# Kernel optimization log

Hardware: AMD Instinct MI355X
Metric: run time of the kernel (lower is better)

## Reference

```python
import jax, jax.numpy as jnp
import numpy as np

CHANNELS = 64
WEIGHT_NUMS = [66 * 64, 64 * 64, 64]  # layer0 (C+2)->C, layer1 C->C, layer2 C->1
BIAS_NUMS = [64, 64, 1]
NUM_GEN_PARAMS = sum(WEIGHT_NUMS) + sum(BIAS_NUMS)  # 8513


def setup_inputs() -> dict:
    key = jax.random.key(0)
    k1, k2 = jax.random.split(key)
    N, C, H, W = 4, 64, 80, 200
    num_ins = 8  # instances per image -> M = 32 total
    M = N * num_ins
    x = jax.random.normal(k1, (N, C, H, W), dtype=jnp.float32)
    mask_head_params = jax.random.normal(k2, (M, NUM_GEN_PARAMS), dtype=jnp.float32) * 0.1
    return {"x": x, "mask_head_params": mask_head_params, "num_ins": num_ins}


def reference(x, mask_head_params, num_ins):
    N, C, H, W = x.shape
    ch = CHANNELS
    # compute_locations with stride=1 (stride//2 == 0); source bug divides the
    # whole tensor by W (locations[:1,:,:] /= W on a batch-1 tensor).
    xx, yy = jnp.meshgrid(jnp.arange(W, dtype=x.dtype), jnp.arange(H, dtype=x.dtype), indexing='xy')
    loc = jnp.stack([xx, yy], axis=0) / W  # [2, H, W]
    xa = jnp.concatenate([jnp.broadcast_to(loc[None], (N, 2, H, W)), x], axis=1)  # [N, C+2, H, W]
    feats = jnp.repeat(xa, num_ins, axis=0)  # [M, C+2, H, W] per-instance inputs
    M = feats.shape[0]
    # parse_dynamic_params: split generated params into per-layer weights/biases
    splits = np.cumsum(WEIGHT_NUMS + BIAS_NUMS)[:-1]
    w0, w1, w2, b0, b1, b2 = jnp.split(mask_head_params, splits, axis=1)
    w0 = w0.reshape(M, ch, ch + 2)
    w1 = w1.reshape(M, ch, ch)
    w2 = w2.reshape(M, 1, ch)
    b2 = b2 - 2.19  # mask bias shift (is_mask=True)
    # grouped 1x1 convs (groups=M) as per-instance GEMMs with ReLU between layers
    h = jax.nn.relu(jnp.einsum('mkc,mchw->mkhw', w0, feats) + b0[:, :, None, None])
    h = jax.nn.relu(jnp.einsum('mkc,mchw->mkhw', w1, h) + b1[:, :, None, None])
    out = jnp.einsum('mkc,mchw->mkhw', w2, h) + b2[:, :, None, None]
    return out.reshape(1, -1, H, W)  # [1, M*out_channels, H, W]
```

## Files before the change

### kernel.cpp

```cpp
#include <hip/hip_runtime.h>

typedef __attribute__((ext_vector_type(8)))  short    short8;
typedef __attribute__((ext_vector_type(4)))  short    s16x4;
typedef __attribute__((ext_vector_type(4)))  float    f32x4;
typedef __attribute__((ext_vector_type(4)))  unsigned uint4_;
typedef __attribute__((ext_vector_type(2)))  unsigned uint2_;

#define HW     16000
#define WWID   200
#define NPARAM 8513
#define PACK_STRIDE 6144

__device__ __forceinline__ unsigned pkbf2(float a, float b) {
    unsigned r;
    asm("v_cvt_pk_bf16_f32 %0, %1, %2" : "=v"(r) : "v"(a), "v"(b));
    return r;
}
__device__ __forceinline__ s16x4 mk4(unsigned a, unsigned b) {
    uint2_ u; u.x = a; u.y = b;
    return __builtin_bit_cast(s16x4, u);
}
__device__ __forceinline__ void mfma16(f32x4& acc, s16x4 a, s16x4 b) {
    asm("s_nop 2\n\tv_mfma_f32_16x16x16_bf16 %0, %1, %2, %0"
        : "+v"(acc) : "v"(a), "v"(b));
}

__device__ __forceinline__ float w0val(const float* pm, int k, int c) {
    if (c < 64)  return pm[k * 66 + c + 2];
    if (c == 64) return pm[k * 66 + 0];
    if (c == 65) return pm[k * 66 + 1];
    if (c == 66) return pm[8384 + k];
    return 0.0f;
}

__global__ __launch_bounds__(256) void pack_weights(
    const float* __restrict__ params, unsigned* __restrict__ wp)
{
    const int m   = blockIdx.x;
    const int tid = threadIdx.x;
    const float* pm = params + (size_t)m * NPARAM;
    unsigned* dst = wp + (size_t)m * PACK_STRIDE;

    if (blockIdx.y == 0) {
        const int l  = tid >> 2;
        const int i0 = (tid & 3) * 2;
        #pragma unroll
        for (int frag = 0; frag < 12; ++frag) {
            int ch = frag >> 2, kb = frag & 3;
            int k = kb * 16 + (l & 15);
            int c = ch * 32 + (l >> 4) * 8 + i0;
            dst[frag * 256 + tid] = pkbf2(w0val(pm, k, c), w0val(pm, k, c + 1));
        }
        float* fd = (float*)dst;
        if (tid < 64) {
            fd[5120 + tid] = pm[8448 + tid];
            fd[5184 + tid] = pm[8320 + tid];
        }
        if (tid == 0) fd[5248] = pm[8512];
    } else {
        #pragma unroll
        for (int i = tid; i < 2048; i += 256) {
            int f = i >> 7, r = i & 127;
            int l = r >> 1, d = i & 1;
            int kb = f >> 2, ks = f & 3;
            int row = kb * 16 + (l & 15);
            int col = ks * 16 + (l >> 4) * 4 + d * 2;
            const float* s = pm + 4224 + row * 64 + col;
            dst[3072 + i] = pkbf2(s[0], s[1]);
        }
    }
}

__global__ __launch_bounds__(512, 4) void condlane_reg(
    const float* __restrict__ x,
    const unsigned* __restrict__ wp,
    float* __restrict__ out,
    int num_ins)
{
    extern __shared__ char lds_[];
    char*  xt = lds_;
    float* sm = (float*)(lds_ + 32768);
    const int tid  = threadIdx.x;
    const int lane = tid & 63;
    const int wid  = tid >> 6;
    const int n    = blockIdx.y;
    const int pxg0 = blockIdx.x * 128;
    const int g    = (lane >> 4) & 3;
    const int px16 = lane & 15;

    {
        const int p   = tid & 127;
        const int sel = tid >> 7;
        const float* xp = x + (size_t)n * 64 * HW + (pxg0 + p);
        #pragma unroll
        for (int it = 0; it < 2; ++it) {
            int c0 = sel * 16 + it * 8;
            uint4_ d;
            d.x = pkbf2(xp[(size_t)(c0 + 0) * HW], xp[(size_t)(c0 + 1) * HW]);
            d.y = pkbf2(xp[(size_t)(c0 + 2) * HW], xp[(size_t)(c0 + 3) * HW]);
            d.z = pkbf2(xp[(size_t)(c0 + 4) * HW], xp[(size_t)(c0 + 5) * HW]);
            d.w = pkbf2(xp[(size_t)(c0 + 6) * HW], xp[(size_t)(c0 + 7) * HW]);
            *(uint4_*)(xt + ((p * 256 + c0 * 2) ^ ((p & 15) << 4))) = d;
        }
        const int pg = pxg0 + p;
        float lx = (float)(pg % WWID) * (1.0f / WWID);
        float ly = (float)(pg / WWID) * (1.0f / WWID);
        uint4_ cv;
        cv.x = (sel == 0) ? pkbf2(lx, ly)   : 0u;
        cv.y = (sel == 0) ? pkbf2(1.f, 0.f) : 0u;
        cv.z = 0u; cv.w = 0u;
        *(uint4_*)(xt + ((p * 256 + 128 + sel * 16) ^ ((p & 15) << 4))) = cv;
    }

    const int m = n * num_ins + wid;
    const unsigned* wm = wp + (size_t)m * PACK_STRIDE;
    const float*    fm = (const float*)wm;
    float* sw = sm + wid * 136;

    sw[lane]      = fm[5120 + lane];
    sw[64 + lane] = fm[5184 + lane];
    if (lane == 0) sw[128] = fm[5248];

    short8 w0f[3][4];
    s16x4  w1f4[4][4];
    #pragma unroll
    for (int ch = 0; ch < 3; ++ch)
        #pragma unroll
        for (int kb = 0; kb < 4; ++kb)
            w0f[ch][kb] = *(const short8*)(wm + (ch * 4 + kb) * 256 + lane * 4);
    #pragma unroll
    for (int kb = 0; kb < 4; ++kb)
        #pragma unroll
        for (int ks = 0; ks < 4; ++ks)
            w1f4[kb][ks] = *(const s16x4*)(wm + 3072 + (kb * 4 + ks) * 128 + lane * 2);

    __syncthreads();

    const int swz = px16 << 4;
    const float* swg = sw + g * 4;

    for (int s = 0; s < 8; ++s) {
        const int pxl = s * 16 + px16;
        short8 xf[3];
        #pragma unroll
        for (int ch = 0; ch < 3; ++ch)
            xf[ch] = *(const short8*)(xt + ((pxl * 256 + ch * 64 + g * 16) ^ swz));
        f32x4 zero4; zero4[0] = 0.f; zero4[1] = 0.f; zero4[2] = 0.f; zero4[3] = 0.f;
        f32x4 acc0[4];
        #pragma unroll
        for (int kb = 0; kb < 4; ++kb)
            acc0[kb] = __builtin_amdgcn_mfma_f32_16x16x32_bf16(w0f[0][kb], xf[0], zero4, 0, 0, 0);
        #pragma unroll
        for (int ch = 1; ch < 3; ++ch)
            #pragma unroll
            for (int kb = 0; kb < 4; ++kb)
                acc0[kb] = __builtin_amdgcn_mfma_f32_16x16x32_bf16(w0f[ch][kb], xf[ch], acc0[kb], 0, 0, 0);
        s16x4 hf[4];
        #pragma unroll
        for (int ks = 0; ks < 4; ++ks)
            hf[ks] = mk4(pkbf2(fmaxf(acc0[ks][0], 0.f), fmaxf(acc0[ks][1], 0.f)),
                         pkbf2(fmaxf(acc0[ks][2], 0.f), fmaxf(acc0[ks][3], 0.f)));
        f32x4 acc1[4];
        #pragma unroll
        for (int kb = 0; kb < 4; ++kb)
            acc1[kb] = *(const f32x4*)(swg + kb * 16);
        #pragma unroll
        for (int ks = 0; ks < 4; ++ks)
            #pragma unroll
            for (int kb = 0; kb < 4; ++kb)
                mfma16(acc1[kb], w1f4[kb][ks], hf[ks]);
        asm("s_nop 7\n\ts_nop 7"
            : "+v"(acc1[0]), "+v"(acc1[1]), "+v"(acc1[2]), "+v"(acc1[3]));
        float v = 0.f;
        #pragma unroll
        for (int kb = 0; kb < 4; ++kb) {
            f32x4 w2k = *(const f32x4*)(swg + 64 + kb * 16);
            #pragma unroll
            for (int r = 0; r < 4; ++r)
                v += w2k[r] * fmaxf(acc1[kb][r], 0.f);
        }
        v += __shfl_xor(v, 16);
        v += __shfl_xor(v, 32);
        if (lane < 16)
            out[(size_t)m * HW + pxg0 + s * 16 + lane] = v + (sw[128] - 2.19f);
    }
}

extern "C" void kernel_launch(void* const* d_in, const int* in_sizes, int n_in,
                              void* d_out, int out_size, void* d_ws, size_t ws_size,
                              hipStream_t stream) {
    const float* x      = (const float*)d_in[0];
    const float* params = (const float*)d_in[1];
    float* out          = (float*)d_out;

    const int N = in_sizes[0] / (64 * HW);
    const int M = in_sizes[1] / NPARAM;
    const int num_ins = M / N;

    pack_weights<<<dim3(M, 2), 256, 0, stream>>>(params, (unsigned*)d_ws);

    dim3 grid(HW / 128, N);
    condlane_reg<<<grid, 512, 37120, stream>>>(x, (const unsigned*)d_ws, out, num_ins);
}
```

Baseline: 28.78 us.

## Fold location/bias channels into small K=16 MFMA and shrink LDS tile

Drops the third 32-wide K chunk of layer 0, which held only the two coordinate channels and the bias. Those are now handled by four 16x16x16 MFMAs whose B operand (x/y location, 1.0) is built in registers each step. The x tile in LDS halves to 128 bytes per pixel with a narrower swizzle, and the packed weight layout shrinks to match. This cuts LDS footprint, LDS writes and layer-0 MFMA work, which may raise occupancy. The cost is extra nop padding and per-step coordinate arithmetic.

```diff
diff --git a/kernel.cpp b/kernel.cpp
--- a/kernel.cpp
+++ b/kernel.cpp
@@ -9,7 +9,7 @@
 #define HW     16000
 #define WWID   200
 #define NPARAM 8513
-#define PACK_STRIDE 6144
+#define PACK_STRIDE 4864
 
 __device__ __forceinline__ unsigned pkbf2(float a, float b) {
     unsigned r;
@@ -24,13 +24,9 @@
     asm("s_nop 2\n\tv_mfma_f32_16x16x16_bf16 %0, %1, %2, %0"
         : "+v"(acc) : "v"(a), "v"(b));
 }
-
-__device__ __forceinline__ float w0val(const float* pm, int k, int c) {
-    if (c < 64)  return pm[k * 66 + c + 2];
-    if (c == 64) return pm[k * 66 + 0];
-    if (c == 65) return pm[k * 66 + 1];
-    if (c == 66) return pm[8384 + k];
-    return 0.0f;
+__device__ __forceinline__ void mfma16c(f32x4& acc, s16x4 a, s16x4 b) {
+    asm("s_nop 7\n\tv_mfma_f32_16x16x16_bf16 %0, %1, %2, %0"
+        : "+v"(acc) : "v"(a), "v"(b));
 }
 
 __global__ __launch_bounds__(256) void pack_weights(
@@ -45,18 +41,32 @@
         const int l  = tid >> 2;
         const int i0 = (tid & 3) * 2;
         #pragma unroll
-        for (int frag = 0; frag < 12; ++frag) {
-            int ch = frag >> 2, kb = frag & 3;
+        for (int f = 0; f < 8; ++f) {
+            int ch = f >> 2, kb = f & 3;
             int k = kb * 16 + (l & 15);
             int c = ch * 32 + (l >> 4) * 8 + i0;
-            dst[frag * 256 + tid] = pkbf2(w0val(pm, k, c), w0val(pm, k, c + 1));
+            const float* s = pm + k * 66 + 2 + c;
+            dst[f * 256 + tid] = pkbf2(s[0], s[1]);
+        }
+        #pragma unroll
+        for (int it = 0; it < 2; ++it) {
+            int idx = it * 256 + tid;
+            int kb = idx >> 7, rem = idx & 127;
+            int ll = rem >> 1, d = rem & 1;
+            int gg = (ll >> 4) & 3;
+            int k = kb * 16 + (ll & 15);
+            unsigned v = 0u;
+            if (gg == 0)
+                v = d ? pkbf2(pm[8384 + k], 0.f)
+                      : pkbf2(pm[k * 66 + 0], pm[k * 66 + 1]);
+            dst[4096 + idx] = v;
         }
         float* fd = (float*)dst;
         if (tid < 64) {
-            fd[5120 + tid] = pm[8448 + tid];
-            fd[5184 + tid] = pm[8320 + tid];
-        }
-        if (tid == 0) fd[5248] = pm[8512];
+            fd[4608 + tid] = pm[8448 + tid];
+            fd[4672 + tid] = pm[8320 + tid];
+        }
+        if (tid == 0) fd[4736] = pm[8512];
     } else {
         #pragma unroll
         for (int i = tid; i < 2048; i += 256) {
@@ -66,7 +76,7 @@
             int row = kb * 16 + (l & 15);
             int col = ks * 16 + (l >> 4) * 4 + d * 2;
             const float* s = pm + 4224 + row * 64 + col;
-            dst[3072 + i] = pkbf2(s[0], s[1]);
+            dst[2048 + i] = pkbf2(s[0], s[1]);
         }
     }
 }
@@ -79,7 +89,7 @@
 {
     extern __shared__ char lds_[];
     char*  xt = lds_;
-    float* sm = (float*)(lds_ + 32768);
+    float* sm = (float*)(lds_ + 16384);
     const int tid  = threadIdx.x;
     const int lane = tid & 63;
     const int wid  = tid >> 6;
@@ -100,16 +110,8 @@
             d.y = pkbf2(xp[(size_t)(c0 + 2) * HW], xp[(size_t)(c0 + 3) * HW]);
             d.z = pkbf2(xp[(size_t)(c0 + 4) * HW], xp[(size_t)(c0 + 5) * HW]);
             d.w = pkbf2(xp[(size_t)(c0 + 6) * HW], xp[(size_t)(c0 + 7) * HW]);
-            *(uint4_*)(xt + ((p * 256 + c0 * 2) ^ ((p & 15) << 4))) = d;
-        }
-        const int pg = pxg0 + p;
-        float lx = (float)(pg % WWID) * (1.0f / WWID);
-        float ly = (float)(pg / WWID) * (1.0f / WWID);
-        uint4_ cv;
-        cv.x = (sel == 0) ? pkbf2(lx, ly)   : 0u;
-        cv.y = (sel == 0) ? pkbf2(1.f, 0.f) : 0u;
-        cv.z = 0u; cv.w = 0u;
-        *(uint4_*)(xt + ((p * 256 + 128 + sel * 16) ^ ((p & 15) << 4))) = cv;
+            *(uint4_*)(xt + ((p * 128 + c0 * 2) ^ ((p & 7) << 4))) = d;
+        }
     }
 
     const int m = n * num_ins + wid;
@@ -117,44 +119,65 @@
     const float*    fm = (const float*)wm;
     float* sw = sm + wid * 136;
 
-    sw[lane]      = fm[5120 + lane];
-    sw[64 + lane] = fm[5184 + lane];
-    if (lane == 0) sw[128] = fm[5248];
-
-    short8 w0f[3][4];
+    sw[lane]      = fm[4608 + lane];
+    sw[64 + lane] = fm[4672 + lane];
+    if (lane == 0) sw[128] = fm[4736];
+
+    short8 w0f[2][4];
     s16x4  w1f4[4][4];
+    s16x4  wloc[4];
     #pragma unroll
-    for (int ch = 0; ch < 3; ++ch)
+    for (int ch = 0; ch < 2; ++ch)
         #pragma unroll
         for (int kb = 0; kb < 4; ++kb)
             w0f[ch][kb] = *(const short8*)(wm + (ch * 4 + kb) * 256 + lane * 4);
     #pragma unroll
-    for (int kb = 0; kb < 4; ++kb)
+    for (int kb = 0; kb < 4; ++kb) {
         #pragma unroll
         for (int ks = 0; ks < 4; ++ks)
-            w1f4[kb][ks] = *(const s16x4*)(wm + 3072 + (kb * 4 + ks) * 128 + lane * 2);
+            w1f4[kb][ks] = *(const s16x4*)(wm + 2048 + (kb * 4 + ks) * 128 + lane * 2);
+        wloc[kb] = *(const s16x4*)(wm + 4096 + kb * 128 + lane * 2);
+    }
+
+    const int pxg00 = pxg0 + px16;
+    float colf = (float)(pxg00 % WWID);
+    float rowf = (float)(pxg00 / WWID);
+    const unsigned gmask = (g == 0) ? 0xFFFFFFFFu : 0u;
+    const unsigned lbv   = (g == 0) ? 0x00003f80u : 0u;
 
     __syncthreads();
 
-    const int swz = px16 << 4;
+    const int swz = (px16 & 7) << 4;
     const float* swg = sw + g * 4;
 
     for (int s = 0; s < 8; ++s) {
         const int pxl = s * 16 + px16;
-        short8 xf[3];
-        #pragma unroll
-        for (int ch = 0; ch < 3; ++ch)
-            xf[ch] = *(const short8*)(xt + ((pxl * 256 + ch * 64 + g * 16) ^ swz));
+        short8 xf[2];
+        #pragma unroll
+        for (int ch = 0; ch < 2; ++ch)
+            xf[ch] = *(const short8*)(xt + ((pxl * 128 + ch * 64 + g * 16) ^ swz));
         f32x4 zero4; zero4[0] = 0.f; zero4[1] = 0.f; zero4[2] = 0.f; zero4[3] = 0.f;
         f32x4 acc0[4];
         #pragma unroll
         for (int kb = 0; kb < 4; ++kb)
             acc0[kb] = __builtin_amdgcn_mfma_f32_16x16x32_bf16(w0f[0][kb], xf[0], zero4, 0, 0, 0);
         #pragma unroll
-        for (int ch = 1; ch < 3; ++ch)
+        for (int kb = 0; kb < 4; ++kb)
+            acc0[kb] = __builtin_amdgcn_mfma_f32_16x16x32_bf16(w0f[1][kb], xf[1], acc0[kb], 0, 0, 0);
+        {
+            float lx = colf * (1.0f / WWID);
+            float ly = rowf * (1.0f / WWID);
+            s16x4 locB = mk4(pkbf2(lx, ly) & gmask, lbv);
             #pragma unroll
             for (int kb = 0; kb < 4; ++kb)
-                acc0[kb] = __builtin_amdgcn_mfma_f32_16x16x32_bf16(w0f[ch][kb], xf[ch], acc0[kb], 0, 0, 0);
+                mfma16c(acc0[kb], wloc[kb], locB);
+            colf += 16.f;
+            bool wrap = colf >= (float)WWID;
+            colf = wrap ? colf - (float)WWID : colf;
+            rowf = wrap ? rowf + 1.f : rowf;
+        }
+        asm("s_nop 7\n\ts_nop 7"
+            : "+v"(acc0[0]), "+v"(acc0[1]), "+v"(acc0[2]), "+v"(acc0[3]));
         s16x4 hf[4];
         #pragma unroll
         for (int ks = 0; ks < 4; ++ks)
@@ -200,5 +223,5 @@
     pack_weights<<<dim3(M, 2), 256, 0, stream>>>(params, (unsigned*)d_ws);
 
     dim3 grid(HW / 128, N);
-    condlane_reg<<<grid, 512, 37120, stream>>>(x, (const unsigned*)d_ws, out, num_ins);
-}
+    condlane_reg<<<grid, 512, 20736, stream>>>(x, (const unsigned*)d_ws, out, num_ins);
+}
```

Result: no change. 28.76 us (-0.1%).
